# Performance work log

Hardware: AMD Instinct MI355X
Metric: run time of the kernel (lower is better)

Reference implementation:

```python
import jax, jax.numpy as jnp
import numpy as np

TOP_K = 2


def setup_inputs() -> dict:
    key = jax.random.key(0)
    k1, k2, k3, k4, k5 = jax.random.split(key, 5)
    H, F, E = 1024, 2048, 8
    B, S = 2, 1024
    return {
        "hidden_states": jax.random.normal(k1, (B, S, H), dtype=jnp.float32),
        "gate_w": jax.random.normal(k2, (E, H), dtype=jnp.float32) * (1.0 / np.sqrt(H)),
        "w1": jax.random.normal(k3, (E, F, H), dtype=jnp.float32) * (1.0 / np.sqrt(H)),
        "w2": jax.random.normal(k4, (E, H, F), dtype=jnp.float32) * (1.0 / np.sqrt(F)),
        "w3": jax.random.normal(k5, (E, F, H), dtype=jnp.float32) * (1.0 / np.sqrt(H)),
    }


def reference(hidden_states, gate_w, w1, w2, w3):
    B, S, H = hidden_states.shape
    E = gate_w.shape[0]
    x = hidden_states.reshape(-1, H)  # [T, H]

    # Router: softmax in float32, top-k, renormalize (exact Mixtral math)
    router_logits = x @ gate_w.T  # [T, E]
    probs = jax.nn.softmax(router_logits.astype(jnp.float32), axis=-1)
    routing_weights, selected = jax.lax.top_k(probs, TOP_K)  # [T, K]
    routing_weights = routing_weights / routing_weights.sum(axis=-1, keepdims=True)
    routing_weights = routing_weights.astype(x.dtype)

    # Per-token combine weight for each expert: [T, E]
    combine = (jax.nn.one_hot(selected, E, dtype=x.dtype) * routing_weights[..., None]).sum(axis=1)

    # Dense grouped expert SwiGLU MLP (zero combine weight for unselected experts
    # makes this strictly equivalent to the gathered/dispatched computation)
    h = jnp.einsum('th,efh->etf', x, w1)   # [E, T, F]
    g = jnp.einsum('th,efh->etf', x, w3)   # [E, T, F]
    mid = jax.nn.silu(h) * g               # SwiGLU
    expert_out = jnp.einsum('etf,ehf->eth', mid, w2)  # [E, T, H]
    out = jnp.einsum('eth,te->th', expert_out, combine)  # weighted combine

    return out.reshape(B, S, H), router_logits
```

## Files before the change

kernel.cpp:

```cpp
#include <hip/hip_runtime.h>
#include <hip/hip_bf16.h>
#include <math.h>

#define H 1024
#define FF 2048
#define E 8
#define T 2048
#define NSLOT (2*T)
#define SLOT_PAD 128

#define WELEM (E*FF*H)
#define XELEM (T*H)
#define WCONV_BLKS 6144
#define CONV_BLKS 6400

typedef __attribute__((ext_vector_type(8))) short s16x8;
typedef __attribute__((ext_vector_type(4))) float f32x4;
typedef __attribute__((ext_vector_type(4))) unsigned int u32x4;

static __device__ __forceinline__ unsigned short f2bf(float f) {
    union { float f; unsigned u; } v; v.f = f;
    unsigned r = v.u + 0x7fff + ((v.u >> 16) & 1);
    return (unsigned short)(r >> 16);
}
static __device__ __forceinline__ float bf2f(unsigned short s) {
    union { unsigned u; float f; } v; v.u = ((unsigned)s) << 16;
    return v.f;
}
static __device__ __forceinline__ unsigned pack2(float a, float b) {
    return (unsigned)f2bf(a) | ((unsigned)f2bf(b) << 16);
}

typedef __attribute__((address_space(3))) unsigned int lds_uint;
typedef const __attribute__((address_space(1))) unsigned int glob_uint;
static __device__ __forceinline__ void gl_lds16(const void* g, void* l) {
    __builtin_amdgcn_global_load_lds((glob_uint*)g, (lds_uint*)l, 16, 0, 0);
}

static __device__ __forceinline__ void expert_range(const int* __restrict__ counts,
                                                    int e, int& off, int& cnt) {
    int acc = 0;
    #pragma unroll
    for (int i = 0; i < E; ++i) {
        int c = counts[i];
        if (i < e) acc += c;
        if (i == e) cnt = c;
    }
    off = acc;
}

__global__ __launch_bounds__(256) void conv_kernel(
    const float* __restrict__ w1, const float* __restrict__ w3,
    const float* __restrict__ w2, const float* __restrict__ x,
    unsigned short* __restrict__ w1b, unsigned short* __restrict__ w3b,
    unsigned short* __restrict__ w2b, unsigned short* __restrict__ xb)
{
    int b = blockIdx.x, tid = threadIdx.x;
    int r = b >> 11;
    const float* s = (r == 0) ? w1 : (r == 1) ? w3 : (r == 2) ? w2 : x;
    unsigned short* d = (r == 0) ? w1b : (r == 1) ? w3b : (r == 2) ? w2b : xb;
    size_t base = (size_t)(b & 2047) * 8192;

    f32x4 a[8];
    #pragma unroll
    for (int j = 0; j < 8; ++j)
        a[j] = __builtin_nontemporal_load((const f32x4*)(s + base + (size_t)(j * 256 + tid) * 4));
    #pragma unroll
    for (int j = 0; j < 8; ++j) {
        uint2 rr;
        rr.x = pack2(a[j].x, a[j].y);
        rr.y = pack2(a[j].z, a[j].w);
        *(uint2*)(d + base + (size_t)(j * 256 + tid) * 4) = rr;
    }
}

__global__ __launch_bounds__(256) void router_kernel(
    const float* __restrict__ x, const float* __restrict__ gw,
    float* __restrict__ logits_out, int* __restrict__ top_id,
    float* __restrict__ top_w, int* __restrict__ counts)
{
    int t = blockIdx.x;
    int tid = threadIdx.x;
    int e = tid >> 5;
    int l32 = tid & 31;
    const float* xr = x + (size_t)t * H;
    const float* gr = gw + (size_t)e * H;
    float s = 0.f;
    for (int h = l32; h < H; h += 32) s += xr[h] * gr[h];
    for (int off = 16; off; off >>= 1) s += __shfl_down(s, off, 32);
    __shared__ float lg[E];
    if (l32 == 0) lg[e] = s;
    __syncthreads();
    if (tid < E) logits_out[(size_t)t * E + tid] = lg[tid];
    if (tid == 0) {
        int i1 = 0; float b1 = lg[0];
        for (int i = 1; i < E; ++i) if (lg[i] > b1) { b1 = lg[i]; i1 = i; }
        int i2 = -1; float b2 = -INFINITY;
        for (int i = 0; i < E; ++i) if (i != i1 && lg[i] > b2) { b2 = lg[i]; i2 = i; }
        float p2 = expf(b2 - b1);
        float inv = 1.f / (1.f + p2);
        top_id[2*t]   = i1;  top_id[2*t+1] = i2;
        top_w[2*t]    = inv; top_w[2*t+1]  = p2 * inv;
        atomicAdd(&counts[i1], 1);
        atomicAdd(&counts[i2], 1);
    }
}

__global__ __launch_bounds__(256) void assign_kernel(
    const int* __restrict__ top_id, const int* __restrict__ counts,
    int* __restrict__ cursors, int* __restrict__ top_pos,
    int* __restrict__ slot_token)
{
    int t = blockIdx.x * 256 + threadIdx.x;
    if (t >= T) return;
    int offs[E];
    {
        int acc = 0;
        #pragma unroll
        for (int i = 0; i < E; ++i) { offs[i] = acc; acc += counts[i]; }
    }
    #pragma unroll
    for (int k = 0; k < 2; ++k) {
        int e = top_id[2*t + k];
        int p = offs[e] + atomicAdd(&cursors[e], 1);
        top_pos[2*t + k] = p;
        slot_token[p] = t;
    }
}

__global__ __launch_bounds__(256) void gemm1_kernel(
    const unsigned short* __restrict__ xb, const int* __restrict__ slot_token,
    const unsigned short* __restrict__ w1b, const unsigned short* __restrict__ w3b,
    const int* __restrict__ counts, unsigned short* __restrict__ mid)
{
    int e = blockIdx.z;
    int off, cnt;
    expert_range(counts, e, off, cnt);
    int m0 = blockIdx.y * 128;
    if (m0 >= cnt) return;
    int f0 = blockIdx.x * 128;

    __shared__ __align__(16) unsigned short sx[128 * 64];
    __shared__ __align__(16) unsigned short s1[128 * 64];
    __shared__ __align__(16) unsigned short s3[128 * 64];

    int tid = threadIdx.x;
    int wv = tid >> 6, ln = tid & 63;
    int quad = ln >> 4, l16 = ln & 15;
    int wm = wv & 1, wn = wv >> 1;
    int xor7 = l16 & 7;

    const unsigned short* xsrc[4]; unsigned short* xdst[4];
    #pragma unroll
    for (int j = 0; j < 4; ++j) {
        int row = wv * 32 + j * 8 + (ln >> 3);
        int slot = off + m0 + row;
        if (m0 + row >= cnt) slot = off;
        int tok = slot_token[slot];
        int cl = (ln & 7) ^ (row & 7);
        xsrc[j] = xb + (size_t)tok * H + cl * 8;
        xdst[j] = &sx[(wv * 32 + j * 8) * 64];
    }
    const unsigned short *w1s[4], *w3s[4]; unsigned short *d1[4], *d3[4];
    #pragma unroll
    for (int j = 0; j < 4; ++j) {
        int row = wv * 32 + j * 8 + (ln >> 3);
        int cl = (ln & 7) ^ (row & 7);
        w1s[j] = w1b + ((size_t)e * FF + f0 + row) * H + cl * 8;
        w3s[j] = w3b + ((size_t)e * FF + f0 + row) * H + cl * 8;
        d1[j] = &s1[(wv * 32 + j * 8) * 64];
        d3[j] = &s3[(wv * 32 + j * 8) * 64];
    }

    f32x4 acc1[4][4], acc3[4][4];
    #pragma unroll
    for (int i = 0; i < 4; ++i)
        #pragma unroll
        for (int j = 0; j < 4; ++j) {
            acc1[i][j] = (f32x4){0.f, 0.f, 0.f, 0.f};
            acc3[i][j] = (f32x4){0.f, 0.f, 0.f, 0.f};
        }

    for (int k0 = 0; k0 < H; k0 += 64) {
        #pragma unroll
        for (int j = 0; j < 4; ++j) {
            gl_lds16(xsrc[j] + k0, xdst[j]);
            gl_lds16(w1s[j] + k0, d1[j]);
            gl_lds16(w3s[j] + k0, d3[j]);
        }
        __syncthreads();
        #pragma unroll
        for (int ks = 0; ks < 2; ++ks) {
            int cph = ((quad + 4 * ks) ^ xor7) << 3;
            s16x8 a[4], b1v[4], b3v[4];
            #pragma unroll
            for (int i = 0; i < 4; ++i)
                a[i] = *(const s16x8*)&sx[(wm * 64 + i * 16 + l16) * 64 + cph];
            #pragma unroll
            for (int j = 0; j < 4; ++j) {
                b1v[j] = *(const s16x8*)&s1[(wn * 64 + j * 16 + l16) * 64 + cph];
                b3v[j] = *(const s16x8*)&s3[(wn * 64 + j * 16 + l16) * 64 + cph];
            }
            #pragma unroll
            for (int i = 0; i < 4; ++i)
                #pragma unroll
                for (int j = 0; j < 4; ++j) {
                    acc1[i][j] = __builtin_amdgcn_mfma_f32_16x16x32_bf16(a[i], b1v[j], acc1[i][j], 0, 0, 0);
                    acc3[i][j] = __builtin_amdgcn_mfma_f32_16x16x32_bf16(a[i], b3v[j], acc3[i][j], 0, 0, 0);
                }
        }
        __syncthreads();
    }

    #pragma unroll
    for (int i = 0; i < 4; ++i) {
        #pragma unroll
        for (int r = 0; r < 4; ++r) {
            int row = wm * 64 + i * 16 + quad * 4 + r;
            if (m0 + row < cnt) {
                size_t base = (size_t)(off + m0 + row) * FF + f0 + wn * 64;
                #pragma unroll
                for (int j = 0; j < 4; ++j) {
                    float h = acc1[i][j][r];
                    float g = acc3[i][j][r];
                    float v = h / (1.f + __expf(-h)) * g;
                    mid[base + j * 16 + l16] = f2bf(v);
                }
            }
        }
    }
}

__global__ __launch_bounds__(256) void gemm2_kernel(
    const unsigned short* __restrict__ mid, const unsigned short* __restrict__ w2b,
    const int* __restrict__ counts, unsigned short* __restrict__ y)
{
    int e = blockIdx.z;
    int off, cnt;
    expert_range(counts, e, off, cnt);
    int m0 = blockIdx.y * 128;
    if (m0 >= cnt) return;
    int n0 = blockIdx.x * 128;

    __shared__ __align__(16) unsigned short sa[128 * 64];
    __shared__ __align__(16) unsigned short sb[128 * 64];

    int tid = threadIdx.x;
    int wv = tid >> 6, ln = tid & 63;
    int quad = ln >> 4, l16 = ln & 15;
    int wm = wv & 1, wn = wv >> 1;
    int xor7 = l16 & 7;

    const unsigned short* asrc[4]; unsigned short* adst[4];
    #pragma unroll
    for (int j = 0; j < 4; ++j) {
        int row = wv * 32 + j * 8 + (ln >> 3);
        int cl = (ln & 7) ^ (row & 7);
        asrc[j] = mid + (size_t)(off + m0 + row) * FF + cl * 8;
        adst[j] = &sa[(wv * 32 + j * 8) * 64];
    }
    const unsigned short* bsrc[4]; unsigned short* bdst[4];
    #pragma unroll
    for (int j = 0; j < 4; ++j) {
        int row = wv * 32 + j * 8 + (ln >> 3);
        int cl = (ln & 7) ^ (row & 7);
        bsrc[j] = w2b + ((size_t)e * H + n0 + row) * FF + cl * 8;
        bdst[j] = &sb[(wv * 32 + j * 8) * 64];
    }

    f32x4 acc[4][4];
    #pragma unroll
    for (int i = 0; i < 4; ++i)
        #pragma unroll
        for (int j = 0; j < 4; ++j) acc[i][j] = (f32x4){0.f, 0.f, 0.f, 0.f};

    for (int k0 = 0; k0 < FF; k0 += 64) {
        #pragma unroll
        for (int j = 0; j < 4; ++j) {
            gl_lds16(asrc[j] + k0, adst[j]);
            gl_lds16(bsrc[j] + k0, bdst[j]);
        }
        __syncthreads();
        #pragma unroll
        for (int ks = 0; ks < 2; ++ks) {
            int cph = ((quad + 4 * ks) ^ xor7) << 3;
            s16x8 a[4], b[4];
            #pragma unroll
            for (int i = 0; i < 4; ++i)
                a[i] = *(const s16x8*)&sa[(wm * 64 + i * 16 + l16) * 64 + cph];
            #pragma unroll
            for (int j = 0; j < 4; ++j)
                b[j] = *(const s16x8*)&sb[(wn * 64 + j * 16 + l16) * 64 + cph];
            #pragma unroll
            for (int i = 0; i < 4; ++i)
                #pragma unroll
                for (int j = 0; j < 4; ++j)
                    acc[i][j] = __builtin_amdgcn_mfma_f32_16x16x32_bf16(a[i], b[j], acc[i][j], 0, 0, 0);
        }
        __syncthreads();
    }

    #pragma unroll
    for (int i = 0; i < 4; ++i) {
        #pragma unroll
        for (int r = 0; r < 4; ++r) {
            int row = wm * 64 + i * 16 + quad * 4 + r;
            if (m0 + row < cnt) {
                size_t base = (size_t)(off + m0 + row) * H + n0 + wn * 64;
                #pragma unroll
                for (int j = 0; j < 4; ++j)
                    y[base + j * 16 + l16] = f2bf(acc[i][j][r]);
            }
        }
    }
}

__global__ __launch_bounds__(256) void combine_kernel(
    const unsigned short* __restrict__ y, const int* __restrict__ top_pos,
    const float* __restrict__ top_w, float* __restrict__ out)
{
    int t = blockIdx.x, tid = threadIdx.x;
    int p0 = top_pos[2*t], p1 = top_pos[2*t+1];
    float w0 = top_w[2*t], w1 = top_w[2*t+1];
    ushort4 a = ((const ushort4*)(y + (size_t)p0 * H))[tid];
    ushort4 b = ((const ushort4*)(y + (size_t)p1 * H))[tid];
    float4 o;
    o.x = w0 * bf2f(a.x) + w1 * bf2f(b.x);
    o.y = w0 * bf2f(a.y) + w1 * bf2f(b.y);
    o.z = w0 * bf2f(a.z) + w1 * bf2f(b.z);
    o.w = w0 * bf2f(a.w) + w1 * bf2f(b.w);
    ((float4*)(out + (size_t)t * H))[tid] = o;
}

extern "C" void kernel_launch(void* const* d_in, const int* in_sizes, int n_in,
                              void* d_out, int out_size, void* d_ws, size_t ws_size,
                              hipStream_t stream) {
    const float* x  = (const float*)d_in[0];
    const float* gw = (const float*)d_in[1];
    const float* w1 = (const float*)d_in[2];
    const float* w2 = (const float*)d_in[3];
    const float* w3 = (const float*)d_in[4];
    float* out    = (float*)d_out;
    float* logits = out + (size_t)T * H;

    int* counts      = (int*)d_ws;
    int* cursors     = counts + 8;
    int* top_id      = counts + 16;
    int* top_pos     = top_id + 2*T;
    int* slot_token  = top_pos + 2*T;
    float* top_w     = (float*)(slot_token + NSLOT);
    unsigned short* xb  = (unsigned short*)(top_w + 2*T);
    unsigned short* mid = xb  + (size_t)T * H;
    unsigned short* y   = mid + (size_t)(NSLOT + SLOT_PAD) * FF;
    unsigned short* w1b = y   + (size_t)NSLOT * H;
    unsigned short* w3b = w1b + (size_t)WELEM;
    unsigned short* w2b = w3b + (size_t)WELEM;

    (void)hipMemsetAsync(counts, 0, 16 * sizeof(int), stream);

    conv_kernel<<<CONV_BLKS, 256, 0, stream>>>(w1, w3, w2, x, w1b, w3b, w2b, xb);
    router_kernel<<<T, 256, 0, stream>>>(x, gw, logits, top_id, top_w, counts);
    assign_kernel<<<(T + 255) / 256, 256, 0, stream>>>(top_id, counts, cursors,
                                                       top_pos, slot_token);
    gemm1_kernel<<<dim3(FF / 128, 16, E), 256, 0, stream>>>(xb, slot_token,
                                                            w1b, w3b, counts, mid);
    gemm2_kernel<<<dim3(H / 128, 16, E), 256, 0, stream>>>(mid, w2b, counts, y);
    combine_kernel<<<T, 256, 0, stream>>>(y, top_pos, top_w, out);
}
```

Before: 429.7 us.

## Drop separate weight conversion pass; load fp32 weights and convert in GEMM

Removes the standalone kernel that converted all expert weights and activations to bf16. The GEMM kernels now stream fp32 weight tiles straight into LDS and convert them to bf16 with packed convert instructions just before the MFMA. Activation conversion moves into the router kernel. This avoids one full read of the fp32 weights plus the bf16 write and re-read. In exchange, the GEMMs load twice the weight bytes per tile, use more LDS (which can lower occupancy), and spend extra ALU on conversion inside the inner loop.

```diff
diff --git a/kernel.cpp b/kernel.cpp
--- a/kernel.cpp
+++ b/kernel.cpp
@@ -9,11 +9,6 @@
 #define NSLOT (2*T)
 #define SLOT_PAD 128
 
-#define WELEM (E*FF*H)
-#define XELEM (T*H)
-#define WCONV_BLKS 6144
-#define CONV_BLKS 6400
-
 typedef __attribute__((ext_vector_type(8))) short s16x8;
 typedef __attribute__((ext_vector_type(4))) float f32x4;
 typedef __attribute__((ext_vector_type(4))) unsigned int u32x4;
@@ -31,6 +26,15 @@
     return (unsigned)f2bf(a) | ((unsigned)f2bf(b) << 16);
 }
 
+static __device__ __forceinline__ s16x8 cvt8(f32x4 lo, f32x4 hi) {
+    union { u32x4 u; s16x8 s; } r;
+    asm("v_cvt_pk_bf16_f32 %0, %1, %2" : "=v"(r.u.x) : "v"(lo.x), "v"(lo.y));
+    asm("v_cvt_pk_bf16_f32 %0, %1, %2" : "=v"(r.u.y) : "v"(lo.z), "v"(lo.w));
+    asm("v_cvt_pk_bf16_f32 %0, %1, %2" : "=v"(r.u.z) : "v"(hi.x), "v"(hi.y));
+    asm("v_cvt_pk_bf16_f32 %0, %1, %2" : "=v"(r.u.w) : "v"(hi.z), "v"(hi.w));
+    return r.s;
+}
+
 typedef __attribute__((address_space(3))) unsigned int lds_uint;
 typedef const __attribute__((address_space(1))) unsigned int glob_uint;
 static __device__ __forceinline__ void gl_lds16(const void* g, void* l) {
@@ -49,41 +53,22 @@
     off = acc;
 }
 
-__global__ __launch_bounds__(256) void conv_kernel(
-    const float* __restrict__ w1, const float* __restrict__ w3,
-    const float* __restrict__ w2, const float* __restrict__ x,
-    unsigned short* __restrict__ w1b, unsigned short* __restrict__ w3b,
-    unsigned short* __restrict__ w2b, unsigned short* __restrict__ xb)
-{
-    int b = blockIdx.x, tid = threadIdx.x;
-    int r = b >> 11;
-    const float* s = (r == 0) ? w1 : (r == 1) ? w3 : (r == 2) ? w2 : x;
-    unsigned short* d = (r == 0) ? w1b : (r == 1) ? w3b : (r == 2) ? w2b : xb;
-    size_t base = (size_t)(b & 2047) * 8192;
-
-    f32x4 a[8];
-    #pragma unroll
-    for (int j = 0; j < 8; ++j)
-        a[j] = __builtin_nontemporal_load((const f32x4*)(s + base + (size_t)(j * 256 + tid) * 4));
-    #pragma unroll
-    for (int j = 0; j < 8; ++j) {
-        uint2 rr;
-        rr.x = pack2(a[j].x, a[j].y);
-        rr.y = pack2(a[j].z, a[j].w);
-        *(uint2*)(d + base + (size_t)(j * 256 + tid) * 4) = rr;
-    }
-}
-
 __global__ __launch_bounds__(256) void router_kernel(
     const float* __restrict__ x, const float* __restrict__ gw,
+    unsigned short* __restrict__ xb,
     float* __restrict__ logits_out, int* __restrict__ top_id,
     float* __restrict__ top_w, int* __restrict__ counts)
 {
     int t = blockIdx.x;
     int tid = threadIdx.x;
+    const float* xr = x + (size_t)t * H;
+    {
+        f32x4 v = *(const f32x4*)(xr + tid * 4);
+        uint2 rr; rr.x = pack2(v.x, v.y); rr.y = pack2(v.z, v.w);
+        *(uint2*)(xb + (size_t)t * H + tid * 4) = rr;
+    }
     int e = tid >> 5;
     int l32 = tid & 31;
-    const float* xr = x + (size_t)t * H;
     const float* gr = gw + (size_t)e * H;
     float s = 0.f;
     for (int h = l32; h < H; h += 32) s += xr[h] * gr[h];
@@ -130,7 +115,7 @@
 
 __global__ __launch_bounds__(256) void gemm1_kernel(
     const unsigned short* __restrict__ xb, const int* __restrict__ slot_token,
-    const unsigned short* __restrict__ w1b, const unsigned short* __restrict__ w3b,
+    const float* __restrict__ w1f, const float* __restrict__ w3f,
     const int* __restrict__ counts, unsigned short* __restrict__ mid)
 {
     int e = blockIdx.z;
@@ -141,8 +126,8 @@
     int f0 = blockIdx.x * 128;
 
     __shared__ __align__(16) unsigned short sx[128 * 64];
-    __shared__ __align__(16) unsigned short s1[128 * 64];
-    __shared__ __align__(16) unsigned short s3[128 * 64];
+    __shared__ __align__(16) float s1f[128 * 64];
+    __shared__ __align__(16) float s3f[128 * 64];
 
     int tid = threadIdx.x;
     int wv = tid >> 6, ln = tid & 63;
@@ -161,15 +146,15 @@
         xsrc[j] = xb + (size_t)tok * H + cl * 8;
         xdst[j] = &sx[(wv * 32 + j * 8) * 64];
     }
-    const unsigned short *w1s[4], *w3s[4]; unsigned short *d1[4], *d3[4];
-    #pragma unroll
-    for (int j = 0; j < 4; ++j) {
-        int row = wv * 32 + j * 8 + (ln >> 3);
-        int cl = (ln & 7) ^ (row & 7);
-        w1s[j] = w1b + ((size_t)e * FF + f0 + row) * H + cl * 8;
-        w3s[j] = w3b + ((size_t)e * FF + f0 + row) * H + cl * 8;
-        d1[j] = &s1[(wv * 32 + j * 8) * 64];
-        d3[j] = &s3[(wv * 32 + j * 8) * 64];
+    const float *b1src[8], *b3src[8]; float *b1dst[8], *b3dst[8];
+    #pragma unroll
+    for (int j = 0; j < 8; ++j) {
+        int row = wv * 32 + j * 4 + (ln >> 4);
+        int g = (ln & 15) ^ (row & 15);
+        b1src[j] = w1f + ((size_t)e * FF + f0 + row) * H + g * 4;
+        b3src[j] = w3f + ((size_t)e * FF + f0 + row) * H + g * 4;
+        b1dst[j] = &s1f[(wv * 32 + j * 4) * 64];
+        b3dst[j] = &s3f[(wv * 32 + j * 4) * 64];
     }
 
     f32x4 acc1[4][4], acc3[4][4];
@@ -183,23 +168,29 @@
 
     for (int k0 = 0; k0 < H; k0 += 64) {
         #pragma unroll
-        for (int j = 0; j < 4; ++j) {
-            gl_lds16(xsrc[j] + k0, xdst[j]);
-            gl_lds16(w1s[j] + k0, d1[j]);
-            gl_lds16(w3s[j] + k0, d3[j]);
+        for (int j = 0; j < 4; ++j) gl_lds16(xsrc[j] + k0, xdst[j]);
+        #pragma unroll
+        for (int j = 0; j < 8; ++j) {
+            gl_lds16(b1src[j] + k0, b1dst[j]);
+            gl_lds16(b3src[j] + k0, b3dst[j]);
         }
         __syncthreads();
         #pragma unroll
         for (int ks = 0; ks < 2; ++ks) {
-            int cph = ((quad + 4 * ks) ^ xor7) << 3;
+            int qa  = (quad + 4 * ks) ^ xor7;
+            int cph = qa << 3;
+            int p2  = (quad + 4 * ks) << 1;
             s16x8 a[4], b1v[4], b3v[4];
             #pragma unroll
             for (int i = 0; i < 4; ++i)
                 a[i] = *(const s16x8*)&sx[(wm * 64 + i * 16 + l16) * 64 + cph];
             #pragma unroll
             for (int j = 0; j < 4; ++j) {
-                b1v[j] = *(const s16x8*)&s1[(wn * 64 + j * 16 + l16) * 64 + cph];
-                b3v[j] = *(const s16x8*)&s3[(wn * 64 + j * 16 + l16) * 64 + cph];
+                int rb = (wn * 64 + j * 16 + l16) * 64;
+                int g0 = (p2 ^ l16) << 2;
+                int g1 = ((p2 ^ 1) ^ l16) << 2;
+                b1v[j] = cvt8(*(const f32x4*)&s1f[rb + g0], *(const f32x4*)&s1f[rb + g1]);
+                b3v[j] = cvt8(*(const f32x4*)&s3f[rb + g0], *(const f32x4*)&s3f[rb + g1]);
             }
             #pragma unroll
             for (int i = 0; i < 4; ++i)
@@ -232,7 +223,7 @@
 }
 
 __global__ __launch_bounds__(256) void gemm2_kernel(
-    const unsigned short* __restrict__ mid, const unsigned short* __restrict__ w2b,
+    const unsigned short* __restrict__ mid, const float* __restrict__ w2f,
     const int* __restrict__ counts, unsigned short* __restrict__ y)
 {
     int e = blockIdx.z;
@@ -243,7 +234,7 @@
     int n0 = blockIdx.x * 128;
 
     __shared__ __align__(16) unsigned short sa[128 * 64];
-    __shared__ __align__(16) unsigned short sb[128 * 64];
+    __shared__ __align__(16) float sbf[128 * 64];
 
     int tid = threadIdx.x;
     int wv = tid >> 6, ln = tid & 63;
@@ -259,13 +250,13 @@
         asrc[j] = mid + (size_t)(off + m0 + row) * FF + cl * 8;
         adst[j] = &sa[(wv * 32 + j * 8) * 64];
     }
-    const unsigned short* bsrc[4]; unsigned short* bdst[4];
-    #pragma unroll
-    for (int j = 0; j < 4; ++j) {
-        int row = wv * 32 + j * 8 + (ln >> 3);
-        int cl = (ln & 7) ^ (row & 7);
-        bsrc[j] = w2b + ((size_t)e * H + n0 + row) * FF + cl * 8;
-        bdst[j] = &sb[(wv * 32 + j * 8) * 64];
+    const float* bsrc[8]; float* bdst[8];
+    #pragma unroll
+    for (int j = 0; j < 8; ++j) {
+        int row = wv * 32 + j * 4 + (ln >> 4);
+        int g = (ln & 15) ^ (row & 15);
+        bsrc[j] = w2f + ((size_t)e * H + n0 + row) * FF + g * 4;
+        bdst[j] = &sbf[(wv * 32 + j * 4) * 64];
     }
 
     f32x4 acc[4][4];
@@ -276,21 +267,26 @@
 
     for (int k0 = 0; k0 < FF; k0 += 64) {
         #pragma unroll
-        for (int j = 0; j < 4; ++j) {
-            gl_lds16(asrc[j] + k0, adst[j]);
-            gl_lds16(bsrc[j] + k0, bdst[j]);
-        }
+        for (int j = 0; j < 4; ++j) gl_lds16(asrc[j] + k0, adst[j]);
+        #pragma unroll
+        for (int j = 0; j < 8; ++j) gl_lds16(bsrc[j] + k0, bdst[j]);
         __syncthreads();
         #pragma unroll
         for (int ks = 0; ks < 2; ++ks) {
-            int cph = ((quad + 4 * ks) ^ xor7) << 3;
+            int qa  = (quad + 4 * ks) ^ xor7;
+            int cph = qa << 3;
+            int p2  = (quad + 4 * ks) << 1;
             s16x8 a[4], b[4];
             #pragma unroll
             for (int i = 0; i < 4; ++i)
                 a[i] = *(const s16x8*)&sa[(wm * 64 + i * 16 + l16) * 64 + cph];
             #pragma unroll
-            for (int j = 0; j < 4; ++j)
-                b[j] = *(const s16x8*)&sb[(wn * 64 + j * 16 + l16) * 64 + cph];
+            for (int j = 0; j < 4; ++j) {
+                int rb = (wn * 64 + j * 16 + l16) * 64;
+                int g0 = (p2 ^ l16) << 2;
+                int g1 = ((p2 ^ 1) ^ l16) << 2;
+                b[j] = cvt8(*(const f32x4*)&sbf[rb + g0], *(const f32x4*)&sbf[rb + g1]);
+            }
             #pragma unroll
             for (int i = 0; i < 4; ++i)
                 #pragma unroll
@@ -352,18 +348,14 @@
     unsigned short* xb  = (unsigned short*)(top_w + 2*T);
     unsigned short* mid = xb  + (size_t)T * H;
     unsigned short* y   = mid + (size_t)(NSLOT + SLOT_PAD) * FF;
-    unsigned short* w1b = y   + (size_t)NSLOT * H;
-    unsigned short* w3b = w1b + (size_t)WELEM;
-    unsigned short* w2b = w3b + (size_t)WELEM;
 
     (void)hipMemsetAsync(counts, 0, 16 * sizeof(int), stream);
 
-    conv_kernel<<<CONV_BLKS, 256, 0, stream>>>(w1, w3, w2, x, w1b, w3b, w2b, xb);
-    router_kernel<<<T, 256, 0, stream>>>(x, gw, logits, top_id, top_w, counts);
+    router_kernel<<<T, 256, 0, stream>>>(x, gw, xb, logits, top_id, top_w, counts);
     assign_kernel<<<(T + 255) / 256, 256, 0, stream>>>(top_id, counts, cursors,
                                                        top_pos, slot_token);
     gemm1_kernel<<<dim3(FF / 128, 16, E), 256, 0, stream>>>(xb, slot_token,
-                                                            w1b, w3b, counts, mid);
-    gemm2_kernel<<<dim3(H / 128, 16, E), 256, 0, stream>>>(mid, w2b, counts, y);
+                                                            w1, w3, counts, mid);
+    gemm2_kernel<<<dim3(H / 128, 16, E), 256, 0, stream>>>(mid, w2, counts, y);
     combine_kernel<<<T, 256, 0, stream>>>(y, top_pos, top_w, out);
 }
```

Result: no change. 436.1 us (+1.5%).
